# Kernel tuning notes

Hardware: AMD Instinct MI355X
Metric: run time of the kernel (lower is better)

## Reference

```python
import jax, jax.numpy as jnp
import numpy as np
from jax import lax

T_STEPS = 10       # fixed unroll length in forward (range(10))
TASK = 16          # params['task_size']
FEAT = 256         # input_size - task_size
VOCAB = 128        # params['vocab_size']
SH = 512           # sender_hidden_size
RH = 512           # receiver_hidden_size
ND = 10            # num_digits
B = 16384          # batch_size


def _gru_step(h, x, Wih, Whh, bih, bhh):
    # PyTorch GRU/GRUCell equations. Wih: [3H, In], Whh: [3H, H]
    gi = x @ Wih.T + bih
    gh = h @ Whh.T + bhh
    ir, iz, inn = jnp.split(gi, 3, axis=-1)
    hr, hz, hn = jnp.split(gh, 3, axis=-1)
    r = jax.nn.sigmoid(ir + hr)
    z = jax.nn.sigmoid(iz + hz)
    n = jnp.tanh(inn + r * hn)
    return (1.0 - z) * n + z * h


def setup_inputs() -> dict:
    key = jax.random.key(0)
    ks = jax.random.split(key, 16)
    s = 0.05
    x = jax.random.normal(ks[0], (B, TASK + FEAT), jnp.float32)
    u = jax.random.uniform(ks[1], (T_STEPS, B, VOCAB), jnp.float32, 1e-6, 1.0 - 1e-6)
    gumbel = -jnp.log(-jnp.log(u))  # standard Gumbel noise, fixed for determinism
    inp = {
        "x": x,
        "gumbel": gumbel,
        "W_in": jax.random.normal(ks[2], (SH, FEAT), jnp.float32) * s,
        "b_in": jnp.zeros((SH,), jnp.float32),
        "Wih_s": jax.random.normal(ks[3], (3 * SH, VOCAB), jnp.float32) * s,
        "Whh_s": jax.random.normal(ks[4], (3 * SH, SH), jnp.float32) * s,
        "bih_s": jnp.zeros((3 * SH,), jnp.float32),
        "bhh_s": jnp.zeros((3 * SH,), jnp.float32),
        "W_sp": jax.random.normal(ks[5], (VOCAB, SH), jnp.float32) * s,
        "b_sp": jnp.zeros((VOCAB,), jnp.float32),
        "Wih_r": jax.random.normal(ks[6], (3 * RH, VOCAB), jnp.float32) * s,
        "Whh_r": jax.random.normal(ks[7], (3 * RH, RH), jnp.float32) * s,
        "bih_r": jnp.zeros((3 * RH,), jnp.float32),
        "bhh_r": jnp.zeros((3 * RH,), jnp.float32),
        "W_c": jax.random.normal(ks[8], (ND, RH + TASK), jnp.float32) * s,
        "b_c": jnp.zeros((ND,), jnp.float32),
    }
    return inp


def _forward(x, gumbel, W_in, b_in, Wih_s, Whh_s, bih_s, bhh_s, W_sp, b_sp,
             Wih_r, Whh_r, bih_r, bhh_r, W_c, b_c):
    feats = x[:, TASK:]
    task = x[:, :TASK]
    h0 = jnp.tanh(feats @ W_in.T + b_in)                      # [B, SH]
    inp0 = jnp.zeros((x.shape[0], VOCAB), x.dtype)

    def sender_step(carry, g):
        h, w = carry
        h = _gru_step(h, w, Wih_s, Whh_s, bih_s, bhh_s)
        logits = h @ W_sp.T + b_sp
        y_soft = jax.nn.softmax(logits + g, axis=-1)          # gumbel_softmax, tau=1
        onehot = jax.nn.one_hot(jnp.argmax(y_soft, axis=-1), VOCAB, dtype=y_soft.dtype)
        y = onehot + y_soft - lax.stop_gradient(y_soft)       # hard straight-through
        return (h, lax.stop_gradient(y)), y                   # input_word = y.detach()

    (_, _), output_words = lax.scan(sender_step, (h0, inp0), gumbel)  # [10, B, V]

    # cumulative stop-token masking: once argmax==0 at step i-1, zero all steps >= i
    words = jnp.argmax(output_words, axis=2)                  # [10, B]
    nz = (words != 0).astype(output_words.dtype)
    alive = jnp.concatenate(
        [jnp.ones((1, words.shape[1]), output_words.dtype), jnp.cumprod(nz[:-1], axis=0)],
        axis=0)                                               # [10, B]
    masked = output_words * alive[:, :, None]

    # receiver GRU, zero initial hidden, return final hidden
    hr0 = jnp.zeros((x.shape[0], RH), x.dtype)

    def recv_step(h, w):
        h = _gru_step(h, w, Wih_r, Whh_r, bih_r, bhh_r)
        return h, None

    h_n, _ = lax.scan(recv_step, hr0, masked)                 # [B, RH]
    score = jnp.concatenate([h_n, task], axis=1) @ W_c.T + b_c  # [B, ND]
    return score


def reference(x, gumbel, W_in, b_in, Wih_s, Whh_s, bih_s, bhh_s, W_sp, b_sp,
              Wih_r, Whh_r, bih_r, bhh_r, W_c, b_c):
    return _forward(x, gumbel, W_in, b_in, Wih_s, Whh_s, bih_s, bhh_s, W_sp, b_sp,
                    Wih_r, Whh_r, bih_r, bhh_r, W_c, b_c)
```

## Files before the change

kernel.cpp:

```cpp
#include <hip/hip_runtime.h>
#include <math.h>

#define NB 16384
#define NT 10
#define CHM 8192

typedef _Float16 f16;
typedef f16 f16x8 __attribute__((ext_vector_type(8)));
typedef f16 f16x4 __attribute__((ext_vector_type(4)));
typedef float f32x4 __attribute__((ext_vector_type(4)));

__device__ __forceinline__ float sigm(float v) { return 1.0f / (1.0f + expf(-v)); }
__device__ __forceinline__ float sigm_fast(float v) {
    return __builtin_amdgcn_rcpf(1.0f + __expf(-v));
}
__device__ __forceinline__ float tanh_fast(float v) {
    return 1.0f - 2.0f * __builtin_amdgcn_rcpf(1.0f + __expf(2.0f * v));
}

__device__ __forceinline__ void async_cp16(const f16* g, f16* l) {
    __builtin_amdgcn_global_load_lds(
        (const __attribute__((address_space(1))) unsigned int*)g,
        (__attribute__((address_space(3))) unsigned int*)l, 16, 0, 0);
}

__global__ __launch_bounds__(256) void h0_kernel(
    const float* __restrict__ x, const float* __restrict__ W,
    const float* __restrict__ bias, f16* __restrict__ h_hi, f16* __restrict__ h_lo)
{
    __shared__ __align__(16) float As[32][128];
    __shared__ __align__(16) float Ws[32][64];
    const int t = threadIdx.x;
    const int tx = t & 15, ty = t >> 4;
    const int mBase = blockIdx.x * 128, nBase = blockIdx.y * 64;
    const int kq = (t & 7) * 4, r8 = t >> 3;

    float4 acc[8];
    #pragma unroll
    for (int mi = 0; mi < 8; ++mi) acc[mi] = make_float4(0.f, 0.f, 0.f, 0.f);

    const float* aPtr = x + (size_t)(mBase + r8) * 272 + 16 + kq;
    const float* wPtr = W + (size_t)(nBase + r8) * 256 + kq;

    for (int kb = 0; kb < 8; ++kb) {
        const int k0 = kb * 32;
        __syncthreads();
        #pragma unroll
        for (int i = 0; i < 4; ++i) {
            float4 v = *(const float4*)(aPtr + (size_t)(i * 32) * 272 + k0);
            const int row = r8 + i * 32;
            const float vv[4] = {v.x, v.y, v.z, v.w};
            #pragma unroll
            for (int j = 0; j < 4; ++j) As[kq + j][row ^ ((kq + j) & 28)] = vv[j];
        }
        #pragma unroll
        for (int i = 0; i < 2; ++i) {
            float4 v = *(const float4*)(wPtr + (size_t)(i * 32) * 256 + k0);
            const int row = r8 + i * 32;
            const float vv[4] = {v.x, v.y, v.z, v.w};
            #pragma unroll
            for (int j = 0; j < 4; ++j) Ws[kq + j][row ^ ((kq + j) & 28)] = vv[j];
        }
        __syncthreads();
        #pragma unroll 8
        for (int k = 0; k < 32; ++k) {
            const int s = k & 28;
            float4 a0 = *(const float4*)&As[k][(ty * 8) ^ s];
            float4 a1 = *(const float4*)&As[k][((ty * 8) + 4) ^ s];
            float4 bb = *(const float4*)&Ws[k][(tx * 4) ^ s];
            const float am[8] = {a0.x, a0.y, a0.z, a0.w, a1.x, a1.y, a1.z, a1.w};
            #pragma unroll
            for (int mi = 0; mi < 8; ++mi) {
                acc[mi].x += am[mi] * bb.x; acc[mi].y += am[mi] * bb.y;
                acc[mi].z += am[mi] * bb.z; acc[mi].w += am[mi] * bb.w;
            }
        }
    }
    const int j0 = nBase + tx * 4;
    const int kg = j0 >> 3, jo = j0 & 7;
    const float4 b4 = *(const float4*)&bias[j0];
    #pragma unroll
    for (int mi = 0; mi < 8; ++mi) {
        const int row = mBase + ty * 8 + mi;
        float o[4];
        o[0] = tanhf(acc[mi].x + b4.x); o[1] = tanhf(acc[mi].y + b4.y);
        o[2] = tanhf(acc[mi].z + b4.z); o[3] = tanhf(acc[mi].w + b4.w);
        f16x4 hi4, lo4;
        #pragma unroll
        for (int c = 0; c < 4; ++c) {
            f16 hv = (f16)o[c];
            hi4[c] = hv;
            lo4[c] = (f16)(o[c] - (float)hv);
        }
        *(f16x4*)&h_hi[((size_t)kg * CHM + row) * 8 + jo] = hi4;
        *(f16x4*)&h_lo[((size_t)kg * CHM + row) * 8 + jo] = lo4;
    }
}

__global__ __launch_bounds__(256) void wsplit_kernel(
    const float* __restrict__ W, f16* __restrict__ whi, f16* __restrict__ wlo, int rows)
{
    const int u = blockIdx.x * 256 + threadIdx.x;
    const int kg = u / rows, row = u - kg * rows;
    const float* s = W + (size_t)row * 512 + kg * 8;
    f16x8 hi8, lo8;
    #pragma unroll
    for (int i = 0; i < 8; ++i) {
        float v = s[i];
        f16 hv = (f16)v;
        hi8[i] = hv;
        lo8[i] = (f16)(v - (float)hv);
    }
    *(f16x8*)&whi[(size_t)u * 8] = hi8;
    *(f16x8*)&wlo[(size_t)u * 8] = lo8;
}

__global__ __launch_bounds__(256) void wihT_kernel(
    const float* __restrict__ Wih, float* __restrict__ WihT)
{
    const int u = blockIdx.x * 256 + threadIdx.x;
    const int w = u / 1536, c = u - w * 1536;
    WihT[u] = Wih[(size_t)c * 128 + w];
}

#define INIT_SP() { \
    _Pragma("unroll") \
    for (int i = 0; i < NST; ++i) { \
        const int u = i * 256 + t; \
        const f16* src; \
        if (PURE) { \
            if (u < 512) { \
                src = hc_hi + ((size_t)(u >> 7) * MS + m0 + (u & 127)) * 8; \
            } else { \
                const int w = u - 512; \
                src = w_hi + ((size_t)((w >> 6) & 3) * 1536 + (w >> 8) * 512 + n0 + (w & 63)) * 8; \
            } \
        } else { \
            if (u < 1024) { \
                const int v = u & 511; \
                const f16* hp = (u < 512) ? hc_hi : hc_lo; \
                src = hp + ((size_t)(v >> 7) * MS + m0 + (v & 127)) * 8; \
            } else { \
                const int v = u - 1024; \
                const f16* wp = (v < 768) ? w_hi : w_lo; \
                const int w = (v < 768) ? v : v - 768; \
                src = wp + ((size_t)((w >> 6) & 3) * 1536 + (w >> 8) * 512 + n0 + (w & 63)) * 8; \
            } \
        } \
        sp[i] = src; \
    } \
}
#define STAGE(buf_) { \
    f16* lb_ = lds + ((size_t)(buf_) * UNITS + wbase) * 8; \
    _Pragma("unroll") \
    for (int i = 0; i < NST; ++i) { \
        async_cp16(sp[i], lb_ + (size_t)i * 256 * 8); \
        sp[i] += (i < HCNT) ? (size_t)MS * 32 : (size_t)49152; \
    } \
}

template <int HZERO, int PURE>
__global__ __launch_bounds__(256, 2) void fused_gru(
    const f16* __restrict__ hc_hi, const f16* __restrict__ hc_lo,
    f16* __restrict__ hn_hi, f16* __restrict__ hn_lo,
    const f16* __restrict__ w_hi, const f16* __restrict__ w_lo,
    const float* __restrict__ WihT,
    const float* __restrict__ bih, const float* __restrict__ bhh,
    const int* __restrict__ wsel, int MS)
{
    constexpr int UNITS = PURE ? 1280 : 2560;
    constexpr int NST = PURE ? 5 : 10;
    constexpr int HCNT = PURE ? 2 : 4;
    __shared__ __align__(16) f16 lds[2 * UNITS * 8];
    const int t = threadIdx.x;
    const int lane = t & 63, wave = t >> 6;
    const int wm = wave >> 1, wn = wave & 1;
    const int m0 = blockIdx.x * 128;
    const int n0 = blockIdx.y * 64;
    const int wbase = t & 192;

    const f32x4 z4 = {0.f, 0.f, 0.f, 0.f};
    f32x4 acc[3][4][2];
    #pragma unroll
    for (int g = 0; g < 3; ++g)
        #pragma unroll
        for (int mi = 0; mi < 4; ++mi)
            #pragma unroll
            for (int ni = 0; ni < 2; ++ni) acc[g][mi][ni] = z4;

    if (!HZERO) {
        const int asel = ((lane >> 4) << 7) + wm * 64 + (lane & 15);
        const int bsel = ((lane >> 4) << 6) + wn * 32 + (lane & 15);
        constexpr int B0 = PURE ? 512 : 1024;

        const f16* sp[NST];
        INIT_SP();
        STAGE(0);
        asm volatile("s_waitcnt vmcnt(0)" ::: "memory");
        __syncthreads();

        for (int kb = 0; kb < 16; ++kb) {
            if (kb < 15) STAGE((kb + 1) & 1);

            const f16* lb = lds + (size_t)(kb & 1) * UNITS * 8;
            f16x8 ah[4], al[4];
            #pragma unroll
            for (int mi = 0; mi < 4; ++mi) {
                ah[mi] = *(const f16x8*)&lb[(size_t)(asel + mi * 16) * 8];
                if (!PURE) al[mi] = *(const f16x8*)&lb[(size_t)(512 + asel + mi * 16) * 8];
            }
            #pragma unroll
            for (int g = 0; g < 3; ++g) {
                f16x8 bh[2], bl[2];
                #pragma unroll
                for (int ni = 0; ni < 2; ++ni) {
                    bh[ni] = *(const f16x8*)&lb[(size_t)(B0 + g * 256 + bsel + ni * 16) * 8];
                    if (!PURE) bl[ni] = *(const f16x8*)&lb[(size_t)(1792 + g * 256 + bsel + ni * 16) * 8];
                }
                #pragma unroll
                for (int mi = 0; mi < 4; ++mi)
                    #pragma unroll
                    for (int ni = 0; ni < 2; ++ni) {
                        acc[g][mi][ni] = __builtin_amdgcn_mfma_f32_16x16x32_f16(ah[mi], bh[ni], acc[g][mi][ni], 0, 0, 0);
                        if (!PURE) {
                            acc[g][mi][ni] = __builtin_amdgcn_mfma_f32_16x16x32_f16(ah[mi], bl[ni], acc[g][mi][ni], 0, 0, 0);
                            acc[g][mi][ni] = __builtin_amdgcn_mfma_f32_16x16x32_f16(al[mi], bh[ni], acc[g][mi][ni], 0, 0, 0);
                        }
                    }
            }
            __syncthreads();
        }
    }

    const int colb = n0 + wn * 32 + (lane & 15);
    const int rowb = m0 + wm * 64 + ((lane >> 4) << 2);
    int wd[16];
    #pragma unroll
    for (int mi = 0; mi < 4; ++mi)
        #pragma unroll
        for (int j = 0; j < 4; ++j)
            wd[mi * 4 + j] = wsel ? wsel[rowb + mi * 16 + j] : -1;

    #pragma unroll
    for (int ni = 0; ni < 2; ++ni) {
        const int col = colb + ni * 16;
        const float b_r = bih[col], b_z = bih[512 + col], b_n = bih[1024 + col];
        const float c_r = bhh[col], c_z = bhh[512 + col], c_n = bhh[1024 + col];
        const size_t cbase = (size_t)(col >> 3) * MS * 8 + (col & 7);
        #pragma unroll
        for (int mi = 0; mi < 4; ++mi) {
            #pragma unroll
            for (int j = 0; j < 4; ++j) {
                const int r = rowb + mi * 16 + j;
                const int word = wd[mi * 4 + j];
                float wir = 0.f, wiz = 0.f, win = 0.f;
                if (word >= 0) {
                    const float* wt = WihT + (size_t)word * 1536 + col;
                    wir = wt[0]; wiz = wt[512]; win = wt[1024];
                }
                const size_t idx = cbase + (size_t)r * 8;
                float hold = 0.f;
                if (!HZERO) {
                    hold = (float)hc_hi[idx];
                    if (!PURE) hold += (float)hc_lo[idx];
                }
                const float ra = wir + b_r + acc[0][mi][ni][j] + c_r;
                const float za = wiz + b_z + acc[1][mi][ni][j] + c_z;
                const float rr = PURE ? sigm_fast(ra) : sigm(ra);
                const float zz = PURE ? sigm_fast(za) : sigm(za);
                const float na = win + b_n + rr * (acc[2][mi][ni][j] + c_n);
                const float nn = PURE ? tanh_fast(na) : tanhf(na);
                const float hv = (1.f - zz) * nn + zz * hold;
                const f16 hh = (f16)hv;
                hn_hi[idx] = hh;
                if (!PURE) hn_lo[idx] = (f16)(hv - (float)hh);
            }
        }
    }
}

__global__ __launch_bounds__(256, 2) void argmax_mfma(
    const f16* __restrict__ h0_hi, const f16* __restrict__ h0_lo,
    const f16* __restrict__ h1_hi, const f16* __restrict__ h1_lo,
    const f16* __restrict__ wsp_hi, const f16* __restrict__ wsp_lo,
    const float* __restrict__ bsp, const float* __restrict__ gum,
    int* __restrict__ wout)
{
    __shared__ __align__(16) f16 lds[2 * 1536 * 8];
    const int t = threadIdx.x;
    const int lane = t & 63, wave = t >> 6;
    const int gRow = blockIdx.x * 64;
    const int ch = (gRow >= CHM);
    const int mBase = gRow - ch * CHM;
    const f16* h_hi = ch ? h1_hi : h0_hi;
    const f16* h_lo = ch ? h1_lo : h0_lo;

    const f32x4 z4 = {0.f, 0.f, 0.f, 0.f};
    f32x4 acc[8];
    #pragma unroll
    for (int nf = 0; nf < 8; ++nf) acc[nf] = z4;

    const f16* sp[6];
    sp[0] = h_hi   + ((size_t)(t >> 6) * CHM + mBase + (t & 63)) * 8;
    sp[1] = h_lo   + ((size_t)(t >> 6) * CHM + mBase + (t & 63)) * 8;
    sp[2] = wsp_hi + ((size_t)(t >> 7) * 128 + (t & 127)) * 8;
    sp[3] = wsp_hi + ((size_t)(2 + (t >> 7)) * 128 + (t & 127)) * 8;
    sp[4] = wsp_lo + ((size_t)(t >> 7) * 128 + (t & 127)) * 8;
    sp[5] = wsp_lo + ((size_t)(2 + (t >> 7)) * 128 + (t & 127)) * 8;

    f16x8 st[6];
    #pragma unroll
    for (int i = 0; i < 6; ++i) {
        st[i] = *(const f16x8*)sp[i];
        sp[i] += (i < 2) ? (size_t)CHM * 32 : (size_t)4096;
    }

    const int aselU = (lane >> 4) * 64 + wave * 16 + (lane & 15);
    const int bselU = 512 + (lane >> 4) * 128 + (lane & 15);

    for (int kb = 0; kb < 16; ++kb) {
        f16* lb = lds + (size_t)(kb & 1) * 1536 * 8;
        #pragma unroll
        for (int i = 0; i < 6; ++i)
            *(f16x8*)&lb[(size_t)(i * 256 + t) * 8] = st[i];
        __syncthreads();
        if (kb < 15) {
            #pragma unroll
            for (int i = 0; i < 6; ++i) {
                st[i] = *(const f16x8*)sp[i];
                sp[i] += (i < 2) ? (size_t)CHM * 32 : (size_t)4096;
            }
        }

        f16x8 ah = *(const f16x8*)&lb[(size_t)aselU * 8];
        f16x8 al = *(const f16x8*)&lb[(size_t)(256 + aselU) * 8];
        #pragma unroll
        for (int nf = 0; nf < 8; ++nf) {
            f16x8 bh = *(const f16x8*)&lb[(size_t)(bselU + nf * 16) * 8];
            f16x8 bl = *(const f16x8*)&lb[(size_t)(512 + bselU + nf * 16) * 8];
            acc[nf] = __builtin_amdgcn_mfma_f32_16x16x32_f16(ah, bh, acc[nf], 0, 0, 0);
            acc[nf] = __builtin_amdgcn_mfma_f32_16x16x32_f16(ah, bl, acc[nf], 0, 0, 0);
            acc[nf] = __builtin_amdgcn_mfma_f32_16x16x32_f16(al, bh, acc[nf], 0, 0, 0);
        }
    }

    float bv[4];
    int bi[4];
    #pragma unroll
    for (int j = 0; j < 4; ++j) { bv[j] = -1e30f; bi[j] = 0; }
    const int rw0 = gRow + wave * 16 + ((lane >> 4) << 2);
    #pragma unroll
    for (int nf = 0; nf < 8; ++nf) {
        const int col = (lane & 15) + nf * 16;
        const float bb = bsp[col];
        #pragma unroll
        for (int j = 0; j < 4; ++j) {
            const float v = acc[nf][j] + bb + gum[(size_t)(rw0 + j) * 128 + col];
            if (v > bv[j] || (v == bv[j] && col < bi[j])) { bv[j] = v; bi[j] = col; }
        }
    }
    #pragma unroll
    for (int j = 0; j < 4; ++j) {
        #pragma unroll
        for (int off = 1; off <= 8; off <<= 1) {
            const float ov = __shfl_xor(bv[j], off, 64);
            const int oi = __shfl_xor(bi[j], off, 64);
            if (ov > bv[j] || (ov == bv[j] && oi < bi[j])) { bv[j] = ov; bi[j] = oi; }
        }
        if ((lane & 15) == 0) wout[rw0 + j] = bi[j];
    }
}

__global__ __launch_bounds__(256) void eff_kernel(
    const int* __restrict__ words, int* __restrict__ eff)
{
    const int b = blockIdx.x * 256 + threadIdx.x;
    int alive = 1;
    #pragma unroll
    for (int t = 0; t < NT; ++t) {
        const int w = words[(size_t)t * NB + b];
        eff[(size_t)t * NB + b] = alive ? w : -1;
        alive = alive & (w != 0);
    }
}

__global__ __launch_bounds__(256) void score_kernel(
    const f16* __restrict__ h_hi,
    const float* __restrict__ x, const float* __restrict__ Wc,
    const float* __restrict__ bc, float* __restrict__ out)
{
    __shared__ float Wcs[10][528];
    const int t = threadIdx.x;
    for (int q = t; q < 1320; q += 256)
        *(float4*)&(((float*)Wcs)[q * 4]) = *(const float4*)&Wc[q * 4];
    __syncthreads();

    const int row = blockIdx.x * 256 + t;
    float acc[10];
    #pragma unroll
    for (int d = 0; d < 10; ++d) acc[d] = 0.f;

    for (int kg = 0; kg < 64; ++kg) {
        f16x8 vh = *(const f16x8*)&h_hi[((size_t)kg * NB + row) * 8];
        #pragma unroll
        for (int i = 0; i < 8; ++i) {
            const float v = (float)vh[i];
            #pragma unroll
            for (int d = 0; d < 10; ++d) acc[d] += v * Wcs[d][kg * 8 + i];
        }
    }
    #pragma unroll
    for (int j = 0; j < 16; ++j) {
        const float tv = x[(size_t)row * 272 + j];
        #pragma unroll
        for (int d = 0; d < 10; ++d) acc[d] += tv * Wcs[d][512 + j];
    }
    #pragma unroll
    for (int d = 0; d < 10; ++d) out[(size_t)row * 10 + d] = acc[d] + bc[d];
}

extern "C" void kernel_launch(void* const* d_in, const int* in_sizes, int n_in,
                              void* d_out, int out_size, void* d_ws, size_t ws_size,
                              hipStream_t stream) {
    const float* x      = (const float*)d_in[0];
    const float* gumbel = (const float*)d_in[1];
    const float* W_in   = (const float*)d_in[2];
    const float* b_in   = (const float*)d_in[3];
    const float* Wih_s  = (const float*)d_in[4];
    const float* Whh_s  = (const float*)d_in[5];
    const float* bih_s  = (const float*)d_in[6];
    const float* bhh_s  = (const float*)d_in[7];
    const float* W_sp   = (const float*)d_in[8];
    const float* b_sp   = (const float*)d_in[9];
    const float* Wih_r  = (const float*)d_in[10];
    const float* Whh_r  = (const float*)d_in[11];
    const float* bih_r  = (const float*)d_in[12];
    const float* bhh_r  = (const float*)d_in[13];
    const float* W_c    = (const float*)d_in[14];
    const float* b_c    = (const float*)d_in[15];
    float* out = (float*)d_out;

    char* base = (char*)d_ws;
    f16* cb[3];
    cb[0] = (f16*)(base);
    cb[1] = (f16*)(base + 16777216);
    cb[2] = (f16*)(base + 33554432);
    f16* R0 = (f16*)(base);
    f16* R1 = (f16*)(base + 16777216);
    f16* ws_s_hi = (f16*)(base + 50331648);
    f16* ws_s_lo = (f16*)(base + 51904512);
    f16* ws_r_hi = (f16*)(base + 53477376);
    f16* ws_r_lo = (f16*)(base + 55050240);
    float* wihT_s = (float*)(base + 56623104);
    float* wihT_r = (float*)(base + 57409536);
    int* words   = (int*)(base + 58195968);
    int* eff     = (int*)(base + 58851328);
    f16* wsp_hi  = (f16*)(base + 59506688);
    f16* wsp_lo  = (f16*)(base + 59637760);

    const size_t LOFF = 4194304;
    #define HI(b) (b)
    #define LO(b) ((b) + LOFF)

    const dim3 blk(256);
    const dim3 gFusS(CHM / 128, 8);
    const dim3 gFusR(NB / 128, 8);

    wsplit_kernel<<<dim3(384), blk, 0, stream>>>(Whh_s, ws_s_hi, ws_s_lo, 1536);
    wsplit_kernel<<<dim3(384), blk, 0, stream>>>(Whh_r, ws_r_hi, ws_r_lo, 1536);
    wsplit_kernel<<<dim3(32), blk, 0, stream>>>(W_sp, wsp_hi, wsp_lo, 128);
    wihT_kernel<<<dim3(768), blk, 0, stream>>>(Wih_s, wihT_s);
    wihT_kernel<<<dim3(768), blk, 0, stream>>>(Wih_r, wihT_r);

    h0_kernel<<<gFusS, blk, 0, stream>>>(x, W_in, b_in, HI(cb[0]), LO(cb[0]));
    h0_kernel<<<gFusS, blk, 0, stream>>>(x + (size_t)CHM * 272, W_in, b_in, HI(cb[1]), LO(cb[1]));
    int c0 = 0, c1 = 1, fr = 2;

    for (int t = 0; t < NT; ++t) {
        const int* wprev = (t == 0) ? (const int*)nullptr : (words + (size_t)(t - 1) * NB);
        fused_gru<0, 0><<<gFusS, blk, 0, stream>>>(
            HI(cb[c0]), LO(cb[c0]), HI(cb[fr]), LO(cb[fr]),
            ws_s_hi, ws_s_lo, wihT_s, bih_s, bhh_s, wprev, CHM);
        fused_gru<0, 0><<<gFusS, blk, 0, stream>>>(
            HI(cb[c1]), LO(cb[c1]), HI(cb[c0]), LO(cb[c0]),
            ws_s_hi, ws_s_lo, wihT_s, bih_s, bhh_s,
            wprev ? wprev + CHM : (const int*)nullptr, CHM);
        const int nf = c1; c1 = c0; c0 = fr; fr = nf;
        argmax_mfma<<<dim3(NB / 64), blk, 0, stream>>>(
            HI(cb[c0]), LO(cb[c0]), HI(cb[c1]), LO(cb[c1]), wsp_hi, wsp_lo,
            b_sp, gumbel + (size_t)t * NB * 128, words + (size_t)t * NB);
    }
    eff_kernel<<<dim3(NB / 256), blk, 0, stream>>>(words, eff);

    fused_gru<1, 1><<<gFusR, blk, 0, stream>>>(
        R1, R1, R0, R0, ws_r_hi, ws_r_lo, wihT_r, bih_r, bhh_r, eff, NB);
    for (int t = 1; t < NT; ++t) {
        f16* rin  = (t & 1) ? R0 : R1;
        f16* rout = (t & 1) ? R1 : R0;
        fused_gru<0, 1><<<gFusR, blk, 0, stream>>>(
            rin, rin, rout, rout, ws_r_hi, ws_r_lo, wihT_r, bih_r, bhh_r,
            eff + (size_t)t * NB, NB);
    }

    score_kernel<<<dim3(NB / 256), blk, 0, stream>>>(R1, x, W_c, b_c, out);
}
```

Measured before the change: 1.613 ms.

## Run sender GRU as one full-batch launch with swizzled block order

Replaces the two half-batch sender GRU launches per step (8192 rows each, with a three-buffer rotation) by a single full-batch launch over 16384 rows. Hidden-state buffers now use full-batch strides with separate hi/lo ping-pong buffers, and argmax reads one buffer. Blocks are remapped from a 1D grid so that consecutive blocks cover different row tiles of the same column tile, which is meant to improve cache reuse of the weight slices. This removes launch overhead and tail effects from the split launches, but the workspace grows and the offsets of all other buffers shift.

```diff
diff --git a/kernel.cpp b/kernel.cpp
--- a/kernel.cpp
+++ b/kernel.cpp
@@ -3,7 +3,6 @@
 
 #define NB 16384
 #define NT 10
-#define CHM 8192
 
 typedef _Float16 f16;
 typedef f16 f16x8 __attribute__((ext_vector_type(8)));
@@ -92,8 +91,8 @@
             hi4[c] = hv;
             lo4[c] = (f16)(o[c] - (float)hv);
         }
-        *(f16x4*)&h_hi[((size_t)kg * CHM + row) * 8 + jo] = hi4;
-        *(f16x4*)&h_lo[((size_t)kg * CHM + row) * 8 + jo] = lo4;
+        *(f16x4*)&h_hi[((size_t)kg * NB + row) * 8 + jo] = hi4;
+        *(f16x4*)&h_lo[((size_t)kg * NB + row) * 8 + jo] = lo4;
     }
 }
 
@@ -130,7 +129,7 @@
         const f16* src; \
         if (PURE) { \
             if (u < 512) { \
-                src = hc_hi + ((size_t)(u >> 7) * MS + m0 + (u & 127)) * 8; \
+                src = hc_hi + ((size_t)(u >> 7) * NB + m0 + (u & 127)) * 8; \
             } else { \
                 const int w = u - 512; \
                 src = w_hi + ((size_t)((w >> 6) & 3) * 1536 + (w >> 8) * 512 + n0 + (w & 63)) * 8; \
@@ -139,7 +138,7 @@
             if (u < 1024) { \
                 const int v = u & 511; \
                 const f16* hp = (u < 512) ? hc_hi : hc_lo; \
-                src = hp + ((size_t)(v >> 7) * MS + m0 + (v & 127)) * 8; \
+                src = hp + ((size_t)(v >> 7) * NB + m0 + (v & 127)) * 8; \
             } else { \
                 const int v = u - 1024; \
                 const f16* wp = (v < 768) ? w_hi : w_lo; \
@@ -155,7 +154,7 @@
     _Pragma("unroll") \
     for (int i = 0; i < NST; ++i) { \
         async_cp16(sp[i], lb_ + (size_t)i * 256 * 8); \
-        sp[i] += (i < HCNT) ? (size_t)MS * 32 : (size_t)49152; \
+        sp[i] += (i < HCNT) ? (size_t)NB * 32 : (size_t)49152; \
     } \
 }
 
@@ -166,7 +165,7 @@
     const f16* __restrict__ w_hi, const f16* __restrict__ w_lo,
     const float* __restrict__ WihT,
     const float* __restrict__ bih, const float* __restrict__ bhh,
-    const int* __restrict__ wsel, int MS)
+    const int* __restrict__ wsel)
 {
     constexpr int UNITS = PURE ? 1280 : 2560;
     constexpr int NST = PURE ? 5 : 10;
@@ -175,8 +174,9 @@
     const int t = threadIdx.x;
     const int lane = t & 63, wave = t >> 6;
     const int wm = wave >> 1, wn = wave & 1;
-    const int m0 = blockIdx.x * 128;
-    const int n0 = blockIdx.y * 64;
+    const int nid = (blockIdx.x & 7) * (NB / 128 * 8 / 8) + (blockIdx.x >> 3);
+    const int m0 = (nid >> 3) * 128;
+    const int n0 = (nid & 7) * 64;
     const int wbase = t & 192;
 
     const f32x4 z4 = {0.f, 0.f, 0.f, 0.f};
@@ -246,7 +246,7 @@
         const int col = colb + ni * 16;
         const float b_r = bih[col], b_z = bih[512 + col], b_n = bih[1024 + col];
         const float c_r = bhh[col], c_z = bhh[512 + col], c_n = bhh[1024 + col];
-        const size_t cbase = (size_t)(col >> 3) * MS * 8 + (col & 7);
+        const size_t cbase = (size_t)(col >> 3) * NB * 8 + (col & 7);
         #pragma unroll
         for (int mi = 0; mi < 4; ++mi) {
             #pragma unroll
@@ -280,8 +280,7 @@
 }
 
 __global__ __launch_bounds__(256, 2) void argmax_mfma(
-    const f16* __restrict__ h0_hi, const f16* __restrict__ h0_lo,
-    const f16* __restrict__ h1_hi, const f16* __restrict__ h1_lo,
+    const f16* __restrict__ h_hi, const f16* __restrict__ h_lo,
     const f16* __restrict__ wsp_hi, const f16* __restrict__ wsp_lo,
     const float* __restrict__ bsp, const float* __restrict__ gum,
     int* __restrict__ wout)
@@ -289,11 +288,7 @@
     __shared__ __align__(16) f16 lds[2 * 1536 * 8];
     const int t = threadIdx.x;
     const int lane = t & 63, wave = t >> 6;
-    const int gRow = blockIdx.x * 64;
-    const int ch = (gRow >= CHM);
-    const int mBase = gRow - ch * CHM;
-    const f16* h_hi = ch ? h1_hi : h0_hi;
-    const f16* h_lo = ch ? h1_lo : h0_lo;
+    const int mBase = blockIdx.x * 64;
 
     const f32x4 z4 = {0.f, 0.f, 0.f, 0.f};
     f32x4 acc[8];
@@ -301,8 +296,8 @@
     for (int nf = 0; nf < 8; ++nf) acc[nf] = z4;
 
     const f16* sp[6];
-    sp[0] = h_hi   + ((size_t)(t >> 6) * CHM + mBase + (t & 63)) * 8;
-    sp[1] = h_lo   + ((size_t)(t >> 6) * CHM + mBase + (t & 63)) * 8;
+    sp[0] = h_hi   + ((size_t)(t >> 6) * NB + mBase + (t & 63)) * 8;
+    sp[1] = h_lo   + ((size_t)(t >> 6) * NB + mBase + (t & 63)) * 8;
     sp[2] = wsp_hi + ((size_t)(t >> 7) * 128 + (t & 127)) * 8;
     sp[3] = wsp_hi + ((size_t)(2 + (t >> 7)) * 128 + (t & 127)) * 8;
     sp[4] = wsp_lo + ((size_t)(t >> 7) * 128 + (t & 127)) * 8;
@@ -312,7 +307,7 @@
     #pragma unroll
     for (int i = 0; i < 6; ++i) {
         st[i] = *(const f16x8*)sp[i];
-        sp[i] += (i < 2) ? (size_t)CHM * 32 : (size_t)4096;
+        sp[i] += (i < 2) ? (size_t)NB * 32 : (size_t)4096;
     }
 
     const int aselU = (lane >> 4) * 64 + wave * 16 + (lane & 15);
@@ -328,7 +323,7 @@
             #pragma unroll
             for (int i = 0; i < 6; ++i) {
                 st[i] = *(const f16x8*)sp[i];
-                sp[i] += (i < 2) ? (size_t)CHM * 32 : (size_t)4096;
+                sp[i] += (i < 2) ? (size_t)NB * 32 : (size_t)4096;
             }
         }
 
@@ -348,7 +343,7 @@
     int bi[4];
     #pragma unroll
     for (int j = 0; j < 4; ++j) { bv[j] = -1e30f; bi[j] = 0; }
-    const int rw0 = gRow + wave * 16 + ((lane >> 4) << 2);
+    const int rw0 = mBase + wave * 16 + ((lane >> 4) << 2);
     #pragma unroll
     for (int nf = 0; nf < 8; ++nf) {
         const int col = (lane & 15) + nf * 16;
@@ -441,30 +436,26 @@
     float* out = (float*)d_out;
 
     char* base = (char*)d_ws;
-    f16* cb[3];
-    cb[0] = (f16*)(base);
-    cb[1] = (f16*)(base + 16777216);
-    cb[2] = (f16*)(base + 33554432);
+    f16* S_hi[2], *S_lo[2];
+    S_hi[0] = (f16*)(base);
+    S_lo[0] = (f16*)(base + 16777216);
+    S_hi[1] = (f16*)(base + 33554432);
+    S_lo[1] = (f16*)(base + 50331648);
     f16* R0 = (f16*)(base);
     f16* R1 = (f16*)(base + 16777216);
-    f16* ws_s_hi = (f16*)(base + 50331648);
-    f16* ws_s_lo = (f16*)(base + 51904512);
-    f16* ws_r_hi = (f16*)(base + 53477376);
-    f16* ws_r_lo = (f16*)(base + 55050240);
-    float* wihT_s = (float*)(base + 56623104);
-    float* wihT_r = (float*)(base + 57409536);
-    int* words   = (int*)(base + 58195968);
-    int* eff     = (int*)(base + 58851328);
-    f16* wsp_hi  = (f16*)(base + 59506688);
-    f16* wsp_lo  = (f16*)(base + 59637760);
-
-    const size_t LOFF = 4194304;
-    #define HI(b) (b)
-    #define LO(b) ((b) + LOFF)
+    f16* ws_s_hi = (f16*)(base + 67108864);
+    f16* ws_s_lo = (f16*)(base + 68681728);
+    f16* ws_r_hi = (f16*)(base + 70254592);
+    f16* ws_r_lo = (f16*)(base + 71827456);
+    float* wihT_s = (float*)(base + 73400320);
+    float* wihT_r = (float*)(base + 74186752);
+    int* words   = (int*)(base + 74973184);
+    int* eff     = (int*)(base + 75628544);
+    f16* wsp_hi  = (f16*)(base + 76283904);
+    f16* wsp_lo  = (f16*)(base + 76414976);
 
     const dim3 blk(256);
-    const dim3 gFusS(CHM / 128, 8);
-    const dim3 gFusR(NB / 128, 8);
+    const dim3 gFus(NB / 128 * 8);
 
     wsplit_kernel<<<dim3(384), blk, 0, stream>>>(Whh_s, ws_s_hi, ws_s_lo, 1536);
     wsplit_kernel<<<dim3(384), blk, 0, stream>>>(Whh_r, ws_r_hi, ws_r_lo, 1536);
@@ -472,34 +463,30 @@
     wihT_kernel<<<dim3(768), blk, 0, stream>>>(Wih_s, wihT_s);
     wihT_kernel<<<dim3(768), blk, 0, stream>>>(Wih_r, wihT_r);
 
-    h0_kernel<<<gFusS, blk, 0, stream>>>(x, W_in, b_in, HI(cb[0]), LO(cb[0]));
-    h0_kernel<<<gFusS, blk, 0, stream>>>(x + (size_t)CHM * 272, W_in, b_in, HI(cb[1]), LO(cb[1]));
-    int c0 = 0, c1 = 1, fr = 2;
+    h0_kernel<<<dim3(NB / 128, 8), blk, 0, stream>>>(x, W_in, b_in, S_hi[0], S_lo[0]);
+    int cur = 0;
 
     for (int t = 0; t < NT; ++t) {
         const int* wprev = (t == 0) ? (const int*)nullptr : (words + (size_t)(t - 1) * NB);
-        fused_gru<0, 0><<<gFusS, blk, 0, stream>>>(
-            HI(cb[c0]), LO(cb[c0]), HI(cb[fr]), LO(cb[fr]),
-            ws_s_hi, ws_s_lo, wihT_s, bih_s, bhh_s, wprev, CHM);
-        fused_gru<0, 0><<<gFusS, blk, 0, stream>>>(
-            HI(cb[c1]), LO(cb[c1]), HI(cb[c0]), LO(cb[c0]),
-            ws_s_hi, ws_s_lo, wihT_s, bih_s, bhh_s,
-            wprev ? wprev + CHM : (const int*)nullptr, CHM);
-        const int nf = c1; c1 = c0; c0 = fr; fr = nf;
+        const int nxt = cur ^ 1;
+        fused_gru<0, 0><<<gFus, blk, 0, stream>>>(
+            S_hi[cur], S_lo[cur], S_hi[nxt], S_lo[nxt],
+            ws_s_hi, ws_s_lo, wihT_s, bih_s, bhh_s, wprev);
+        cur = nxt;
         argmax_mfma<<<dim3(NB / 64), blk, 0, stream>>>(
-            HI(cb[c0]), LO(cb[c0]), HI(cb[c1]), LO(cb[c1]), wsp_hi, wsp_lo,
+            S_hi[cur], S_lo[cur], wsp_hi, wsp_lo,
             b_sp, gumbel + (size_t)t * NB * 128, words + (size_t)t * NB);
     }
     eff_kernel<<<dim3(NB / 256), blk, 0, stream>>>(words, eff);
 
-    fused_gru<1, 1><<<gFusR, blk, 0, stream>>>(
-        R1, R1, R0, R0, ws_r_hi, ws_r_lo, wihT_r, bih_r, bhh_r, eff, NB);
+    fused_gru<1, 1><<<gFus, blk, 0, stream>>>(
+        R1, R1, R0, R0, ws_r_hi, ws_r_lo, wihT_r, bih_r, bhh_r, eff);
     for (int t = 1; t < NT; ++t) {
         f16* rin  = (t & 1) ? R0 : R1;
         f16* rout = (t & 1) ? R1 : R0;
-        fused_gru<0, 1><<<gFusR, blk, 0, stream>>>(
+        fused_gru<0, 1><<<gFus, blk, 0, stream>>>(
             rin, rin, rout, rout, ws_r_hi, ws_r_lo, wihT_r, bih_r, bhh_r,
-            eff + (size_t)t * NB, NB);
+            eff + (size_t)t * NB);
     }
 
     score_kernel<<<dim3(NB / 256), blk, 0, stream>>>(R1, x, W_c, b_c, out);
```

After: 1.516 ms. 6.0% less time.
